# Optimization experiments

Measured on AMD Instinct MI355X. Metric: run time of the kernel, lower is better.

Reference implementation:

```python
import jax, jax.numpy as jnp
import numpy as np

V, C, L, D = 16384, 16, 6, 64  # n_vars, max_clauses, max_variables, embedding_dim


def _normalize(x):
    # utils.normalize: L2-normalize along the feature axis
    return x / jnp.linalg.norm(x, axis=-1, keepdims=True)


def _rescombine(x, W1, b1, W2, b2):
    # ResidualCombine: normalize(sigmoid(layer1(x)) + layer2(x))
    h = jax.nn.sigmoid(x @ W1 + b1) + x @ W2 + b2
    return _normalize(h)


def setup_inputs() -> dict:
    key = jax.random.key(0)
    ks = jax.random.split(key, 14)
    s = 0.05
    variables = jax.random.normal(ks[0], (V, D), jnp.float32)
    # literal variable indices; slot 0 of every clause is the owning variable i
    lits = jax.random.randint(ks[1], (V, C, L), 0, V)
    lits = lits.at[:, :, 0].set(jnp.arange(V)[:, None])
    neg_mask = jax.random.bernoulli(ks[2], 0.5, (V, C, L))
    # literal validity: at least 2 literals per clause, slot 0 always valid
    nvar = jax.random.randint(ks[3], (V, C), 2, L + 1)
    var_valid = jnp.arange(L)[None, None, :] < nvar[:, :, None]
    # clause validity: at least 1 clause per variable
    nclause = jax.random.randint(ks[4], (V,), 1, C + 1)
    clause_valid = jnp.arange(C)[None, :] < nclause[:, None]
    # params
    Wn = jax.random.normal(ks[5], (D, D), jnp.float32) * s
    bn = jnp.zeros((D,), jnp.float32)
    f = jax.random.normal(ks[6], (D,), jnp.float32)
    false_emb = f / jnp.linalg.norm(f)  # Embedding(1, D, max_norm=1.0)
    W1v = jax.random.normal(ks[7], (L * D, D), jnp.float32) * s
    b1v = jnp.zeros((D,), jnp.float32)
    W2v = jax.random.normal(ks[8], (L * D, D), jnp.float32) * s
    b2v = jnp.zeros((D,), jnp.float32)
    W1c = jax.random.normal(ks[9], (C * D, D), jnp.float32) * s
    b1c = jnp.zeros((D,), jnp.float32)
    W2c = jax.random.normal(ks[10], (C * D, D), jnp.float32) * s
    b2c = jnp.zeros((D,), jnp.float32)
    return dict(variables=variables, lits=lits, neg_mask=neg_mask, var_valid=var_valid,
                clause_valid=clause_valid, Wn=Wn, bn=bn, false_emb=false_emb,
                W1v=W1v, b1v=b1v, W2v=W2v, b2v=b2v, W1c=W1c, b1c=b1c, W2c=W2c, b2c=b2c)


def reference(variables, lits, neg_mask, var_valid, clause_valid,
              Wn, bn, false_emb, W1v, b1v, W2v, b2v, W1c, b1c, W2c, b2c):
    # gather literal embeddings: [V, C, L, D]
    g = variables[lits]
    # negation linear for negative literals
    v = jnp.where(neg_mask[..., None], g @ Wn + bn, g)
    # pad invalid literal slots with the 'false' embedding
    v = jnp.where(var_valid[..., None], v, false_emb)
    # variable_combiner over flattened [L*D]
    clause_emb = _rescombine(v.reshape(V, C, L * D), W1v, b1v, W2v, b2v)  # [V, C, D]
    # pad missing clauses with 'true' = negation(false)
    true_emb = false_emb @ Wn + bn
    clause_emb = jnp.where(clause_valid[..., None], clause_emb, true_emb)
    # clause_combiner over flattened [C*D]
    out = _rescombine(clause_emb.reshape(V, C * D), W1c, b1c, W2c, b2c)  # [V, D]
    # variables with no clauses pass through unchanged
    has_clauses = clause_valid.any(axis=-1)
    return jnp.where(has_clauses[:, None], out, variables)
```

## Files before the change

### kernel.cpp

```cpp
#include <hip/hip_runtime.h>
#include <hip/hip_bf16.h>

#define NV 16384
#define NC 16
#define NL 6
#define ND 64

typedef unsigned short u16;
typedef unsigned int u32;
typedef __attribute__((ext_vector_type(8))) short short8;
typedef __attribute__((ext_vector_type(4))) float f32x4;

#define PB_BN  0
#define PB_FE  64
#define PB_B1V 128
#define PB_B2V 192
#define PB_B1C 256
#define PB_B2C 320
#define U_BVS   896
#define U_BCS   50048
#define U_BN    181120
#define U_VARSB 185216
#define U_NEGB  1233856
#define U_FIDX  2282496

__device__ __forceinline__ float ldbf(const u16* p, int i) {
  return __uint_as_float(((u32)p[i]) << 16);
}
__device__ __forceinline__ u16 f2b(float f) {
  u32 x = __float_as_uint(f);
  return (u16)((x + 0x7FFF + ((x >> 16) & 1)) >> 16);
}
__device__ __forceinline__ int ldmask(const void* p, int i, int bdt) {
  return bdt ? (int)((const signed char*)p)[i] : ((const int*)p)[i];
}
__device__ __forceinline__ float ldf(const void* p, int i, int fdt) {
  return fdt ? ldbf((const u16*)p, i) : ((const float*)p)[i];
}
__device__ __forceinline__ void gll16(const u16* g, u16* l) {
  __builtin_amdgcn_global_load_lds(
      (const __attribute__((address_space(1))) u32*)(g),
      (__attribute__((address_space(3))) u32*)(l), 16, 0, 0);
}

__global__ __launch_bounds__(256) void k_prep(
    const void* vars, const int* __restrict__ lits, const void* negm, const void* vval,
    const void* Wn, const void* bn, const void* femb,
    const void* W1v, const void* b1v, const void* W2v, const void* b2v,
    const void* W1c, const void* b1c, const void* W2c, const void* b2c,
    int* flags, float* pbuf, u16* wsB) {
  __shared__ int s_cnt[4], s_big[4];
  const int t = threadIdx.x;
  {
    const u32 w = ((const u32*)vars)[t];
    const u32 e = (w >> 7) & 0xFF;
    const unsigned long long bal = __ballot(e >= 0x6E && e <= 0x8E);
    const u32 bw = ((const u32*)vval)[t];
    const unsigned long long bb = __ballot(bw > 1u);
    if ((t & 63) == 0) { s_cnt[t >> 6] = __popcll(bal); s_big[t >> 6] = (bb != 0ull); }
  }
  __syncthreads();
  const int fdt = (s_cnt[0] + s_cnt[1] + s_cnt[2] + s_cnt[3]) >= 192;
  const int bdt = (s_big[0] | s_big[1] | s_big[2] | s_big[3]);
  const int bid = blockIdx.x;

  if (bid == 0) {
    if (t == 0) { flags[0] = fdt; flags[1] = bdt; }
    if (t < 64) {
      const void* src[6] = {bn, femb, b1v, b2v, b1c, b2c};
      const int off[6] = {PB_BN, PB_FE, PB_B1V, PB_B2V, PB_B1C, PB_B2C};
      for (int j = 0; j < 6; j++) pbuf[off[j] + t] = ldf(src[j], t, fdt);
      wsB[U_VARSB + NV * 64 + t] = fdt ? ((const u16*)femb)[t] : f2b(((const float*)femb)[t]);
    }
    for (int i = t; i < 4096; i += 256) {
      const int n = i >> 6, k = i & 63;
      wsB[U_BN + i] = f2b(ldf(Wn, k * 64 + n, fdt));
    }
  } else if (bid < 25) {
    const int c = (bid - 1) * 256 + t;
    const int ln = c & 63, nt = (c >> 6) & 7, ks = c >> 9;
    const int n = nt * 16 + (ln & 15);
    const void* src = (n < 64) ? W1v : W2v;
    const int kb = ks * 32 + (ln >> 4) * 8, n6 = n & 63;
    u16 o[8];
#pragma unroll
    for (int j = 0; j < 8; j++) o[j] = f2b(ldf(src, (kb + j) * 64 + n6, fdt));
    *(short8*)(wsB + U_BVS + c * 8) = *(short8*)o;
  } else if (bid < 89) {
    const int c = (bid - 25) * 256 + t;
    const int ln = c & 63, nt = (c >> 6) & 7, ks = c >> 9;
    const int n = nt * 16 + (ln & 15);
    const void* src = (n < 64) ? W1c : W2c;
    const int kb = ks * 32 + (ln >> 4) * 8, n6 = n & 63;
    u16 o[8];
#pragma unroll
    for (int j = 0; j < 8; j++) o[j] = f2b(ldf(src, (kb + j) * 64 + n6, fdt));
    *(short8*)(wsB + U_BCS + c * 8) = *(short8*)o;
  } else if (bid < 601) {
    const int c8 = (bid - 89) * 256 + t;
    u16 o[8];
    if (fdt) {
      *(short8*)o = ((const short8*)vars)[c8];
    } else {
      const float* f = (const float*)vars + c8 * 8;
#pragma unroll
      for (int j = 0; j < 8; j++) o[j] = f2b(f[j]);
    }
    *(short8*)(wsB + U_VARSB + c8 * 8) = *(short8*)o;
  } else {
    const int i0 = ((bid - 601) * 256 + t) * 4;
    u16 o[4];
#pragma unroll
    for (int j = 0; j < 4; j++) {
      const int i = i0 + j;
      const int valid = ldmask(vval, i, bdt);
      const int neg = ldmask(negm, i, bdt);
      const int idx = lits[i];
      o[j] = (u16)(valid ? (idx + (neg ? (NV + 1) : 0)) : NV);
    }
    *(ushort4*)(wsB + U_FIDX + i0) = *(ushort4*)o;
  }
}

__global__ __launch_bounds__(256) void k_negvar(const float* pbuf, u16* wsB) {
  const int tid = threadIdx.x, lane = tid & 63, wv = tid >> 6;
  const int col = lane & 15, quad = lane >> 4, q8 = quad * 8;
  const int rowbase = blockIdx.x * 64 + wv * 16;
  f32x4 acc[4];
#pragma unroll
  for (int nt = 0; nt < 4; nt++) acc[nt] = (f32x4){0.f, 0.f, 0.f, 0.f};
  const int arow = min(rowbase + col, NV);
#pragma unroll
  for (int ks = 0; ks < 2; ks++) {
    const short8 a = *(const short8*)(wsB + U_VARSB + arow * 64 + ks * 32 + q8);
#pragma unroll
    for (int nt = 0; nt < 4; nt++) {
      const short8 b = *(const short8*)(wsB + U_BN + (nt * 16 + col) * 64 + ks * 32 + q8);
      acc[nt] = __builtin_amdgcn_mfma_f32_16x16x32_bf16(a, b, acc[nt], 0, 0, 0);
    }
  }
#pragma unroll
  for (int reg = 0; reg < 4; reg++) {
    const int r = rowbase + quad * 4 + reg;
    if (r <= NV) {
#pragma unroll
      for (int nt = 0; nt < 4; nt++) {
        const int d = nt * 16 + col;
        wsB[U_NEGB + r * 64 + d] = f2b(acc[nt][reg] + pbuf[PB_BN + d]);
      }
    }
  }
}

__global__ __launch_bounds__(256, 2) void k_main(
    const void* __restrict__ vars, const void* __restrict__ cval,
    const float* __restrict__ pbuf, const int* __restrict__ flags,
    const u16* __restrict__ wsB, void* __restrict__ outv) {
  __shared__ __align__(16) u16 smem[24576];
  __shared__ float ps[16][4];
  __shared__ int hcS[16];

  const int tid = threadIdx.x, lane = tid & 63, wv = tid >> 6;
  const int col = lane & 15, quad = lane >> 4, q8 = quad * 8;
  const int fdt = flags[0], bdt = flags[1];
  const int vbase = (blockIdx.x * 4 + wv) * 4;
  const int v0 = blockIdx.x * 16;

  u32 r2_[4][3];
#pragma unroll
  for (int v4 = 0; v4 < 4; v4++)
#pragma unroll
    for (int i = 0; i < 3; i++)
      r2_[v4][i] = *(const u32*)(wsB + U_FIDX + (vbase + v4) * 96 + col * 6 + i * 2);

  const int cv = ldmask(cval, vbase * 16 + lane, bdt);
  const unsigned long long bal = __ballot(cv != 0);
  if (lane < 4) hcS[wv * 4 + lane] = ((bal >> (lane * 16)) & 0xFFFFull) != 0;

  f32x4 acc[4][8];
#pragma unroll
  for (int v4 = 0; v4 < 4; v4++)
#pragma unroll
    for (int nt = 0; nt < 8; nt++) acc[v4][nt] = (f32x4){0.f, 0.f, 0.f, 0.f};

#pragma unroll
  for (int j = 0; j < 6; j++) {
    const int cl = wv * 6 + j;
    gll16(wsB + U_BVS + cl * 512 + lane * 8, &smem[cl * 512]);
  }
  short8 a_cur[4], a_nxt[4];
#pragma unroll
  for (int v4 = 0; v4 < 4; v4++) {
    const int idx = (int)(r2_[v4][0] & 0xFFFFu);
    a_cur[v4] = *(const short8*)(wsB + U_VARSB + idx * 64 + q8);
  }
  __syncthreads();

  for (int q = 0; q < 4; q++) {
    if (q < 3) {
#pragma unroll
      for (int j = 0; j < 6; j++) {
        const int cl = wv * 6 + j;
        gll16(wsB + U_BVS + (q + 1) * 12288 + cl * 512 + lane * 8,
              &smem[((q + 1) & 1) * 12288 + cl * 512]);
      }
    }
#pragma unroll
    for (int ksl = 0; ksl < 3; ksl++) {
      const int gk = q * 3 + ksl;
      if (gk < 11) {
        const int gn = gk + 1;
        const int goff = (gn & 1) * 32 + q8;
        const int pi = gn >> 2, ph = (gn >> 1) & 1;
#pragma unroll
        for (int v4 = 0; v4 < 4; v4++) {
          const int idx = (int)((r2_[v4][pi] >> (ph * 16)) & 0xFFFFu);
          a_nxt[v4] = *(const short8*)(wsB + U_VARSB + idx * 64 + goff);
        }
      }
#pragma unroll
      for (int nt = 0; nt < 8; nt++) {
        const short8 b = *(const short8*)(&smem[(q & 1) * 12288 + (ksl * 8 + nt) * 512 + lane * 8]);
#pragma unroll
        for (int v4 = 0; v4 < 4; v4++)
          acc[v4][nt] = __builtin_amdgcn_mfma_f32_16x16x32_bf16(a_cur[v4], b, acc[v4][nt], 0, 0, 0);
      }
#pragma unroll
      for (int v4 = 0; v4 < 4; v4++) a_cur[v4] = a_nxt[v4];
    }
    if (q < 3) __syncthreads();
  }
  __syncthreads();

  {
    float b1l[4], b2l[4], truel[4];
#pragma unroll
    for (int nt = 0; nt < 4; nt++) {
      const int d = nt * 16 + col;
      b1l[nt] = pbuf[PB_B1V + d];
      b2l[nt] = pbuf[PB_B2V + d];
      truel[nt] = ldbf(wsB, U_NEGB + NV * 64 + d);
    }
#pragma unroll
    for (int v4 = 0; v4 < 4; v4++) {
      const u32 vmask = (u32)((bal >> (v4 * 16)) & 0xFFFFull);
      const int vloc = wv * 4 + v4;
#pragma unroll
      for (int reg = 0; reg < 4; reg++) {
        const int c = quad * 4 + reg;
        float hh[4], ss = 0.f;
#pragma unroll
        for (int nt = 0; nt < 4; nt++) {
          hh[nt] = 1.0f / (1.0f + __expf(-(acc[v4][nt][reg] + b1l[nt]))) + acc[v4][nt + 4][reg] + b2l[nt];
          ss += hh[nt] * hh[nt];
        }
        ss += __shfl_xor(ss, 1, 64); ss += __shfl_xor(ss, 2, 64);
        ss += __shfl_xor(ss, 4, 64); ss += __shfl_xor(ss, 8, 64);
        const float sc = 1.0f / sqrtf(ss);
        const int valid = (vmask >> c) & 1;
#pragma unroll
        for (int nt = 0; nt < 4; nt++) {
          const float o = valid ? hh[nt] * sc : truel[nt];
          const int l2 = (nt * 2 + (col >> 3)) & 3;
          smem[(c * 2 + (nt >> 1)) * 512 + (l2 * 16 + vloc) * 8 + (col & 7)] = f2b(o);
        }
      }
    }
  }
  __syncthreads();

  f32x4 acc1 = (f32x4){0.f, 0.f, 0.f, 0.f}, acc2 = (f32x4){0.f, 0.f, 0.f, 0.f};
#pragma unroll 8
  for (int ks = 0; ks < 32; ks++) {
    const short8 a = *(const short8*)(&smem[ks * 512 + lane * 8]);
    const short8 b1 = *(const short8*)(wsB + U_BCS + (ks * 8 + wv) * 512 + lane * 8);
    const short8 b2 = *(const short8*)(wsB + U_BCS + (ks * 8 + wv + 4) * 512 + lane * 8);
    acc1 = __builtin_amdgcn_mfma_f32_16x16x32_bf16(a, b1, acc1, 0, 0, 0);
    acc2 = __builtin_amdgcn_mfma_f32_16x16x32_bf16(a, b2, acc2, 0, 0, 0);
  }

  const int d = wv * 16 + col;
  const float b1c_d = pbuf[PB_B1C + d], b2c_d = pbuf[PB_B2C + d];
  float h[4];
#pragma unroll
  for (int reg = 0; reg < 4; reg++) {
    h[reg] = 1.0f / (1.0f + __expf(-(acc1[reg] + b1c_d))) + acc2[reg] + b2c_d;
    float ssp = h[reg] * h[reg];
    ssp += __shfl_xor(ssp, 1, 64); ssp += __shfl_xor(ssp, 2, 64);
    ssp += __shfl_xor(ssp, 4, 64); ssp += __shfl_xor(ssp, 8, 64);
    if (col == 0) ps[quad * 4 + reg][wv] = ssp;
  }
  __syncthreads();
#pragma unroll
  for (int reg = 0; reg < 4; reg++) {
    const int r = quad * 4 + reg;
    const float tot = ps[r][0] + ps[r][1] + ps[r][2] + ps[r][3];
    float o = h[reg] * (1.0f / sqrtf(tot));
    const int oi = (v0 + r) * 64 + d;
    if (hcS[r]) {
      if (fdt) ((u16*)outv)[oi] = f2b(o);
      else ((float*)outv)[oi] = o;
    } else {
      if (fdt) ((u16*)outv)[oi] = ((const u16*)vars)[oi];
      else ((float*)outv)[oi] = ((const float*)vars)[oi];
    }
  }
}

extern "C" void kernel_launch(void* const* d_in, const int* in_sizes, int n_in,
                              void* d_out, int out_size, void* d_ws, size_t ws_size,
                              hipStream_t stream) {
  const void* vars = d_in[0];
  const int* lits = (const int*)d_in[1];
  const void* negm = d_in[2];
  const void* vval = d_in[3];
  const void* cvalid = d_in[4];
  const void* Wn = d_in[5];
  const void* bn = d_in[6];
  const void* femb = d_in[7];
  const void* W1v = d_in[8];
  const void* b1v = d_in[9];
  const void* W2v = d_in[10];
  const void* b2v = d_in[11];
  const void* W1c = d_in[12];
  const void* b1c = d_in[13];
  const void* W2c = d_in[14];
  const void* b2c = d_in[15];

  int* flags = (int*)d_ws;
  float* pbuf = (float*)((char*)d_ws + 256);
  u16* wsB = (u16*)d_ws;

  k_prep<<<2137, 256, 0, stream>>>(vars, lits, negm, vval, Wn, bn, femb,
                                   W1v, b1v, W2v, b2v, W1c, b1c, W2c, b2c,
                                   flags, pbuf, wsB);
  k_negvar<<<(NV + 1 + 63) / 64, 256, 0, stream>>>(pbuf, wsB);
  k_main<<<NV / 16, 256, 0, stream>>>(vars, cvalid, pbuf, flags, wsB, d_out);
}
```

Before: 158.3 us.

## Fold negation matmul into prep kernel and add nontemporal hints and MFMA priority

Removes the separate k_negvar launch and computes the negated-variable table inside extra k_prep blocks. These blocks read raw vars, false_emb and Wn directly, so they no longer depend on the converted bf16 copies written by other prep blocks. This eliminates one kernel launch and its dependency barrier, at the cost of redundant per-block Wn conversion with strided global reads. It also adds nontemporal loads and stores for the index table and output, and raises wave priority around the MFMA loop in k_main.

```diff
diff --git a/kernel.cpp b/kernel.cpp
--- a/kernel.cpp
+++ b/kernel.cpp
@@ -9,6 +9,7 @@
 typedef unsigned short u16;
 typedef unsigned int u32;
 typedef __attribute__((ext_vector_type(8))) short short8;
+typedef __attribute__((ext_vector_type(4))) unsigned short u16x4;
 typedef __attribute__((ext_vector_type(4))) float f32x4;
 
 #define PB_BN  0
@@ -72,10 +73,6 @@
       for (int j = 0; j < 6; j++) pbuf[off[j] + t] = ldf(src[j], t, fdt);
       wsB[U_VARSB + NV * 64 + t] = fdt ? ((const u16*)femb)[t] : f2b(((const float*)femb)[t]);
     }
-    for (int i = t; i < 4096; i += 256) {
-      const int n = i >> 6, k = i & 63;
-      wsB[U_BN + i] = f2b(ldf(Wn, k * 64 + n, fdt));
-    }
   } else if (bid < 25) {
     const int c = (bid - 1) * 256 + t;
     const int ln = c & 63, nt = (c >> 6) & 7, ks = c >> 9;
@@ -107,7 +104,7 @@
       for (int j = 0; j < 8; j++) o[j] = f2b(f[j]);
     }
     *(short8*)(wsB + U_VARSB + c8 * 8) = *(short8*)o;
-  } else {
+  } else if (bid < 2137) {
     const int i0 = ((bid - 601) * 256 + t) * 4;
     u16 o[4];
 #pragma unroll
@@ -118,35 +115,45 @@
       const int idx = lits[i];
       o[j] = (u16)(valid ? (idx + (neg ? (NV + 1) : 0)) : NV);
     }
-    *(ushort4*)(wsB + U_FIDX + i0) = *(ushort4*)o;
-  }
-}
-
-__global__ __launch_bounds__(256) void k_negvar(const float* pbuf, u16* wsB) {
-  const int tid = threadIdx.x, lane = tid & 63, wv = tid >> 6;
-  const int col = lane & 15, quad = lane >> 4, q8 = quad * 8;
-  const int rowbase = blockIdx.x * 64 + wv * 16;
-  f32x4 acc[4];
-#pragma unroll
-  for (int nt = 0; nt < 4; nt++) acc[nt] = (f32x4){0.f, 0.f, 0.f, 0.f};
-  const int arow = min(rowbase + col, NV);
-#pragma unroll
-  for (int ks = 0; ks < 2; ks++) {
-    const short8 a = *(const short8*)(wsB + U_VARSB + arow * 64 + ks * 32 + q8);
-#pragma unroll
-    for (int nt = 0; nt < 4; nt++) {
-      const short8 b = *(const short8*)(wsB + U_BN + (nt * 16 + col) * 64 + ks * 32 + q8);
-      acc[nt] = __builtin_amdgcn_mfma_f32_16x16x32_bf16(a, b, acc[nt], 0, 0, 0);
-    }
-  }
-#pragma unroll
-  for (int reg = 0; reg < 4; reg++) {
-    const int r = rowbase + quad * 4 + reg;
-    if (r <= NV) {
+    u16x4 ov = {o[0], o[1], o[2], o[3]};
+    __builtin_nontemporal_store(ov, (u16x4*)(wsB + U_FIDX + i0));
+  } else {
+    const int nb = bid - 2137;
+    const int lane = t & 63, wv = t >> 6;
+    const int col = lane & 15, quad = lane >> 4, q8 = quad * 8;
+    const int rowbase = nb * 64 + wv * 16;
+    f32x4 acc[4];
+#pragma unroll
+    for (int nt = 0; nt < 4; nt++) acc[nt] = (f32x4){0.f, 0.f, 0.f, 0.f};
+    const int arow = min(rowbase + col, NV);
+#pragma unroll
+    for (int ks = 0; ks < 2; ks++) {
+      short8 a;
+      if (arow == NV) {
+#pragma unroll
+        for (int j = 0; j < 8; j++) a[j] = (short)f2b(ldf(femb, ks * 32 + q8 + j, fdt));
+      } else {
+#pragma unroll
+        for (int j = 0; j < 8; j++) a[j] = (short)f2b(ldf(vars, arow * 64 + ks * 32 + q8 + j, fdt));
+      }
 #pragma unroll
       for (int nt = 0; nt < 4; nt++) {
-        const int d = nt * 16 + col;
-        wsB[U_NEGB + r * 64 + d] = f2b(acc[nt][reg] + pbuf[PB_BN + d]);
+        short8 b;
+#pragma unroll
+        for (int j = 0; j < 8; j++)
+          b[j] = (short)f2b(ldf(Wn, (ks * 32 + q8 + j) * 64 + nt * 16 + col, fdt));
+        acc[nt] = __builtin_amdgcn_mfma_f32_16x16x32_bf16(a, b, acc[nt], 0, 0, 0);
+      }
+    }
+#pragma unroll
+    for (int reg = 0; reg < 4; reg++) {
+      const int r = rowbase + quad * 4 + reg;
+      if (r <= NV) {
+#pragma unroll
+        for (int nt = 0; nt < 4; nt++) {
+          const int d = nt * 16 + col;
+          wsB[U_NEGB + r * 64 + d] = f2b(acc[nt][reg] + ldf(bn, d, fdt));
+        }
       }
     }
   }
@@ -171,7 +178,8 @@
   for (int v4 = 0; v4 < 4; v4++)
 #pragma unroll
     for (int i = 0; i < 3; i++)
-      r2_[v4][i] = *(const u32*)(wsB + U_FIDX + (vbase + v4) * 96 + col * 6 + i * 2);
+      r2_[v4][i] = __builtin_nontemporal_load(
+          (const u32*)(wsB + U_FIDX + (vbase + v4) * 96 + col * 6 + i * 2));
 
   const int cv = ldmask(cval, vbase * 16 + lane, bdt);
   const unsigned long long bal = __ballot(cv != 0);
@@ -218,6 +226,7 @@
           a_nxt[v4] = *(const short8*)(wsB + U_VARSB + idx * 64 + goff);
         }
       }
+      __builtin_amdgcn_s_setprio(1);
 #pragma unroll
       for (int nt = 0; nt < 8; nt++) {
         const short8 b = *(const short8*)(&smem[(q & 1) * 12288 + (ksl * 8 + nt) * 512 + lane * 8]);
@@ -225,6 +234,7 @@
         for (int v4 = 0; v4 < 4; v4++)
           acc[v4][nt] = __builtin_amdgcn_mfma_f32_16x16x32_bf16(a_cur[v4], b, acc[v4][nt], 0, 0, 0);
       }
+      __builtin_amdgcn_s_setprio(0);
 #pragma unroll
       for (int v4 = 0; v4 < 4; v4++) a_cur[v4] = a_nxt[v4];
     }
@@ -298,11 +308,13 @@
     float o = h[reg] * (1.0f / sqrtf(tot));
     const int oi = (v0 + r) * 64 + d;
     if (hcS[r]) {
-      if (fdt) ((u16*)outv)[oi] = f2b(o);
-      else ((float*)outv)[oi] = o;
+      if (fdt) __builtin_nontemporal_store(f2b(o), &((u16*)outv)[oi]);
+      else __builtin_nontemporal_store(o, &((float*)outv)[oi]);
     } else {
-      if (fdt) ((u16*)outv)[oi] = ((const u16*)vars)[oi];
-      else ((float*)outv)[oi] = ((const float*)vars)[oi];
+      if (fdt) __builtin_nontemporal_store(
+          __builtin_nontemporal_load(&((const u16*)vars)[oi]), &((u16*)outv)[oi]);
+      else __builtin_nontemporal_store(
+          __builtin_nontemporal_load(&((const float*)vars)[oi]), &((float*)outv)[oi]);
     }
   }
 }
@@ -331,9 +343,8 @@
   float* pbuf = (float*)((char*)d_ws + 256);
   u16* wsB = (u16*)d_ws;
 
-  k_prep<<<2137, 256, 0, stream>>>(vars, lits, negm, vval, Wn, bn, femb,
+  k_prep<<<2394, 256, 0, stream>>>(vars, lits, negm, vval, Wn, bn, femb,
                                    W1v, b1v, W2v, b2v, W1c, b1c, W2c, b2c,
                                    flags, pbuf, wsB);
-  k_negvar<<<(NV + 1 + 63) / 64, 256, 0, stream>>>(pbuf, wsB);
   k_main<<<NV / 16, 256, 0, stream>>>(vars, cvalid, pbuf, flags, wsB, d_out);
 }
```

After: 156.5 us. No clear change (-1.1%).
